# Kernel optimization log

Hardware: AMD Instinct MI355X
Metric: run time of the kernel (lower is better)

## Reference

```python
import jax, jax.numpy as jnp
import numpy as np

K = 3   # kernel_size
D = 1   # dilation
G = 8   # groups
BN_EPS = 1e-5


def setup_inputs() -> dict:
    key = jax.random.key(0)
    ks = jax.random.split(key, 8)
    N, C, H, W = 8, 64, 256, 256
    k2 = K * K
    x = jax.random.normal(ks[0], (N, C, H, W), jnp.float32)
    conv_w = jax.random.normal(ks[1], (G * k2, C), jnp.float32) * (2.0 / C) ** 0.5
    bn_gamma = jnp.ones((G * k2,), jnp.float32)
    bn_beta = jnp.zeros((G * k2,), jnp.float32)
    bn_mean = jax.random.normal(ks[2], (G * k2,), jnp.float32) * 0.01
    bn_var = jax.random.uniform(ks[3], (G * k2,), jnp.float32, 0.5, 1.5)
    lamb_l = jax.random.normal(ks[4], (C,), jnp.float32) * 0.1
    lamb_h = jax.random.normal(ks[5], (C,), jnp.float32) * 0.1
    inside_all = jax.random.normal(ks[6], (C, 1, 1), jnp.float32) * 0.1
    return {"x": x, "conv_w": conv_w, "bn_gamma": bn_gamma, "bn_beta": bn_beta,
            "bn_mean": bn_mean, "bn_var": bn_var, "lamb_l": lamb_l,
            "lamb_h": lamb_h, "inside_all": inside_all}


def reference(x, conv_w, bn_gamma, bn_beta, bn_mean, bn_var, lamb_l, lamb_h, inside_all):
    N, C, H, W = x.shape
    k2 = K * K
    # ap: adaptive avg pool to (1,1) -> (N, C)
    pooled = x.mean(axis=(2, 3))
    # 1x1 conv on a 1x1 map == matmul; then eval-mode BatchNorm
    lf = pooled @ conv_w.T                                   # (N, G*k2)
    lf = (lf - bn_mean) * (bn_gamma / jnp.sqrt(bn_var + BN_EPS)) + bn_beta
    lf = jnp.tanh(lf).reshape(N, G, 1, k2, 1)                # (N, G, 1, k2, 1)
    # im2col/unfold with reflection padding; ordering matches torch (C, kh, kw)
    p = D * (K - 1) // 2
    xp = jnp.pad(x, ((0, 0), (0, 0), (p, p), (p, p)), mode="reflect")
    patches = jnp.stack(
        [xp[:, :, i * D:i * D + H, j * D:j * D + W] for i in range(K) for j in range(K)],
        axis=2,
    )                                                        # (N, C, k2, H, W)
    xu = patches.reshape(N, G, C // G, k2, H * W)
    low_part = jnp.sum(xu * lf, axis=3).reshape(N, C, H, W)  # per-pixel dynamic filter
    # DSA: gap pools to (1,1)
    gap = x.mean(axis=(2, 3), keepdims=True)                 # (N, C, 1, 1)
    out_low = (low_part * (inside_all + 1.0) - inside_all * gap) * lamb_l[None, :, None, None]
    out_high = x * (lamb_h[None, :, None, None] + 1.0)
    return out_low + out_high
```

## Files before the change

kernel.cpp:

```cpp
#include <hip/hip_runtime.h>
#include <math.h>

#define NN 8
#define CC 64
#define HH 256
#define WW 256
#define GG 8
#define K2 9
#define OC 72
#define BN_EPS 1e-5f

typedef float f4 __attribute__((ext_vector_type(4)));

__global__ __launch_bounds__(1024) void pool_kernel(const float* __restrict__ x,
                                                    float* __restrict__ pooled) {
    int nc = blockIdx.x;
    const f4* p4 = (const f4*)(x + (size_t)nc * (HH * WW));
    float s = 0.f;
#pragma unroll 4
    for (int i = threadIdx.x; i < (HH * WW) / 4; i += 1024) {
        f4 v = p4[i];
        s += (v.x + v.y) + (v.z + v.w);
    }
    for (int off = 32; off > 0; off >>= 1) s += __shfl_down(s, off, 64);
    __shared__ float smem[16];
    int lane = threadIdx.x & 63, wid = threadIdx.x >> 6;
    if (lane == 0) smem[wid] = s;
    __syncthreads();
    if (threadIdx.x < 16) {
        float t = smem[threadIdx.x];
        for (int off = 8; off > 0; off >>= 1) t += __shfl_down(t, off, 64);
        if (threadIdx.x == 0) pooled[nc] = t * (1.0f / (HH * WW));
    }
}

__global__ __launch_bounds__(256) void lf_kernel(const float* __restrict__ pooled,
                                                 const float* __restrict__ conv_w,
                                                 const float* __restrict__ gamma,
                                                 const float* __restrict__ beta,
                                                 const float* __restrict__ mean,
                                                 const float* __restrict__ var,
                                                 float* __restrict__ lf) {
    int j = blockIdx.x * blockDim.x + threadIdx.x;
    if (j >= NN * OC) return;
    int n = j / OC, oc = j % OC;
    const float* pw = conv_w + oc * CC;
    const float* pp = pooled + n * CC;
    float acc = 0.f;
#pragma unroll 8
    for (int c = 0; c < CC; ++c) acc += pp[c] * pw[c];
    float inv = gamma[oc] / sqrtf(var[oc] + BN_EPS);
    lf[j] = tanhf((acc - mean[oc]) * inv + beta[oc]);
}

__global__ __launch_bounds__(256) void main_kernel(const float* __restrict__ x,
                                                   const float* __restrict__ lf,
                                                   const float* __restrict__ pooled,
                                                   const float* __restrict__ lamb_l,
                                                   const float* __restrict__ lamb_h,
                                                   const float* __restrict__ ia,
                                                   float* __restrict__ out) {
    const int bid  = (int)(blockIdx.x & 7) * ((NN * CC * (HH / 32)) >> 3)
                   + (int)(blockIdx.x >> 3);
    const int wid  = threadIdx.x >> 6;
    const int lane = threadIdx.x & 63;
    const int nc   = bid >> 3;
    const int r0   = ((bid & 7) << 5) + (wid << 3);
    const int c    = nc & (CC - 1);
    const int n    = nc >> 6;
    const int g    = c >> 3;

    const float* lw = lf + (n * OC + g * K2);
    const float w00 = lw[0], w01 = lw[1], w02 = lw[2];
    const float w10 = lw[3], w11 = lw[4], w12 = lw[5];
    const float w20 = lw[6], w21 = lw[7], w22 = lw[8];
    const float ll    = lamb_l[c];
    const float lh1   = lamb_h[c] + 1.0f;
    const float iav   = ia[c];
    const float scale = iav + 1.0f;
    const float bias  = -iav * pooled[nc];

    const float* base = x + (size_t)nc * (HH * WW);

    f4    v[10];
    float L[10], R[10];
#pragma unroll
    for (int i = 0; i < 10; ++i) {
        int r = r0 - 1 + i;
        r = (r < 0) ? 1 : ((r > HH - 1) ? HH - 2 : r);
        v[i] = ((const f4*)(base + (size_t)r * WW))[lane];
    }
#pragma unroll
    for (int i = 0; i < 10; ++i) {
        L[i] = __shfl_up(v[i].w, 1, 64);   if (lane == 0)  L[i] = v[i].y;
        R[i] = __shfl_down(v[i].x, 1, 64); if (lane == 63) R[i] = v[i].z;
    }

    float* outbase = out + (size_t)nc * (HH * WW);
#pragma unroll
    for (int j = 0; j < 8; ++j) {
        const float t[6] = {L[j],   v[j].x,   v[j].y,   v[j].z,   v[j].w,   R[j]};
        const float m[6] = {L[j+1], v[j+1].x, v[j+1].y, v[j+1].z, v[j+1].w, R[j+1]};
        const float b[6] = {L[j+2], v[j+2].x, v[j+2].y, v[j+2].z, v[j+2].w, R[j+2]};
        f4 o;
#pragma unroll
        for (int k = 0; k < 4; ++k) {
            float acc = w00 * t[k] + w01 * t[k + 1] + w02 * t[k + 2]
                      + w10 * m[k] + w11 * m[k + 1] + w12 * m[k + 2]
                      + w20 * b[k] + w21 * b[k + 1] + w22 * b[k + 2];
            o[k] = ll * (scale * acc + bias) + lh1 * m[k + 1];
        }
        __builtin_nontemporal_store(o, ((f4*)(outbase + (size_t)(r0 + j) * WW)) + lane);
    }
}

extern "C" void kernel_launch(void* const* d_in, const int* in_sizes, int n_in,
                              void* d_out, int out_size, void* d_ws, size_t ws_size,
                              hipStream_t stream) {
    const float* x      = (const float*)d_in[0];
    const float* conv_w = (const float*)d_in[1];
    const float* gamma  = (const float*)d_in[2];
    const float* beta   = (const float*)d_in[3];
    const float* mean   = (const float*)d_in[4];
    const float* var    = (const float*)d_in[5];
    const float* lamb_l = (const float*)d_in[6];
    const float* lamb_h = (const float*)d_in[7];
    const float* ia     = (const float*)d_in[8];
    float* out = (float*)d_out;

    float* pooled = (float*)d_ws;
    float* lf     = pooled + NN * CC;

    pool_kernel<<<NN * CC, 1024, 0, stream>>>(x, pooled);
    lf_kernel<<<(NN * OC + 255) / 256, 256, 0, stream>>>(pooled, conv_w, gamma, beta,
                                                         mean, var, lf);
    main_kernel<<<NN * CC * (HH / 32), 256, 0, stream>>>(x, lf, pooled, lamb_l, lamb_h,
                                                         ia, out);
}
```

Measured before the change: 264.7 us.

## Fuse pool, filter generation and dynamic conv into one kernel with grid barrier

```diff
diff --git a/kernel.cpp b/kernel.cpp
--- a/kernel.cpp
+++ b/kernel.cpp
@@ -5,112 +5,130 @@
 #define CC 64
 #define HH 256
 #define WW 256
-#define GG 8
 #define K2 9
 #define OC 72
 #define BN_EPS 1e-5f
+#define NBLK (NN * CC * 2)
 
 typedef float f4 __attribute__((ext_vector_type(4)));
 
-__global__ __launch_bounds__(1024) void pool_kernel(const float* __restrict__ x,
-                                                    float* __restrict__ pooled) {
-    int nc = blockIdx.x;
-    const f4* p4 = (const f4*)(x + (size_t)nc * (HH * WW));
-    float s = 0.f;
-#pragma unroll 4
-    for (int i = threadIdx.x; i < (HH * WW) / 4; i += 1024) {
-        f4 v = p4[i];
-        s += (v.x + v.y) + (v.z + v.w);
-    }
-    for (int off = 32; off > 0; off >>= 1) s += __shfl_down(s, off, 64);
-    __shared__ float smem[16];
-    int lane = threadIdx.x & 63, wid = threadIdx.x >> 6;
-    if (lane == 0) smem[wid] = s;
-    __syncthreads();
-    if (threadIdx.x < 16) {
-        float t = smem[threadIdx.x];
-        for (int off = 8; off > 0; off >>= 1) t += __shfl_down(t, off, 64);
-        if (threadIdx.x == 0) pooled[nc] = t * (1.0f / (HH * WW));
-    }
-}
-
-__global__ __launch_bounds__(256) void lf_kernel(const float* __restrict__ pooled,
-                                                 const float* __restrict__ conv_w,
-                                                 const float* __restrict__ gamma,
-                                                 const float* __restrict__ beta,
-                                                 const float* __restrict__ mean,
-                                                 const float* __restrict__ var,
-                                                 float* __restrict__ lf) {
-    int j = blockIdx.x * blockDim.x + threadIdx.x;
-    if (j >= NN * OC) return;
-    int n = j / OC, oc = j % OC;
-    const float* pw = conv_w + oc * CC;
-    const float* pp = pooled + n * CC;
-    float acc = 0.f;
-#pragma unroll 8
-    for (int c = 0; c < CC; ++c) acc += pp[c] * pw[c];
-    float inv = gamma[oc] / sqrtf(var[oc] + BN_EPS);
-    lf[j] = tanhf((acc - mean[oc]) * inv + beta[oc]);
-}
-
-__global__ __launch_bounds__(256) void main_kernel(const float* __restrict__ x,
-                                                   const float* __restrict__ lf,
-                                                   const float* __restrict__ pooled,
-                                                   const float* __restrict__ lamb_l,
-                                                   const float* __restrict__ lamb_h,
-                                                   const float* __restrict__ ia,
-                                                   float* __restrict__ out) {
-    const int bid  = (int)(blockIdx.x & 7) * ((NN * CC * (HH / 32)) >> 3)
-                   + (int)(blockIdx.x >> 3);
+__global__ __launch_bounds__(256, 4) void fused_kernel(
+    const float* __restrict__ x,
+    const float* __restrict__ conv_w,
+    const float* __restrict__ gamma,
+    const float* __restrict__ beta,
+    const float* __restrict__ mean,
+    const float* __restrict__ var,
+    const float* __restrict__ lamb_l,
+    const float* __restrict__ lamb_h,
+    const float* __restrict__ ia,
+    float* __restrict__ out,
+    float* __restrict__ ws,
+    unsigned* __restrict__ sync)
+{
+    const int b    = blockIdx.x;
+    const int nc   = b >> 1;
+    const int half = b & 1;
+    const int lane = threadIdx.x & 63;
     const int wid  = threadIdx.x >> 6;
-    const int lane = threadIdx.x & 63;
-    const int nc   = bid >> 3;
-    const int r0   = ((bid & 7) << 5) + (wid << 3);
     const int c    = nc & (CC - 1);
     const int n    = nc >> 6;
     const int g    = c >> 3;
 
-    const float* lw = lf + (n * OC + g * K2);
-    const float w00 = lw[0], w01 = lw[1], w02 = lw[2];
-    const float w10 = lw[3], w11 = lw[4], w12 = lw[5];
-    const float w20 = lw[6], w21 = lw[7], w22 = lw[8];
+    const float* base  = x + (size_t)nc * (HH * WW);
+    const f4*    hbase = (const f4*)(base + half * (HH / 2) * WW);
+
+    float s = 0.f;
+#pragma unroll 8
+    for (int i = threadIdx.x; i < (HH / 2) * WW / 4; i += 256) {
+        f4 v = hbase[i];
+        s += (v.x + v.y) + (v.z + v.w);
+    }
+    for (int off = 32; off > 0; off >>= 1) s += __shfl_down(s, off, 64);
+    __shared__ float red[4];
+    if (lane == 0) red[wid] = s;
+    __syncthreads();
+    if (threadIdx.x == 0) {
+        float t = (red[0] + red[1]) + (red[2] + red[3]);
+        __hip_atomic_store(&ws[b], t, __ATOMIC_RELEASE, __HIP_MEMORY_SCOPE_AGENT);
+    }
+    __syncthreads();
+
+    if (threadIdx.x == 0) {
+        unsigned prev = __hip_atomic_fetch_add(&sync[0], 1u, __ATOMIC_ACQ_REL,
+                                               __HIP_MEMORY_SCOPE_AGENT);
+        if (prev == NBLK - 1)
+            __hip_atomic_store(&sync[1], 1u, __ATOMIC_RELEASE,
+                               __HIP_MEMORY_SCOPE_AGENT);
+        while (__hip_atomic_load(&sync[1], __ATOMIC_ACQUIRE,
+                                 __HIP_MEMORY_SCOPE_AGENT) == 0u) {
+            __builtin_amdgcn_s_sleep(8);
+        }
+    }
+    __syncthreads();
+
+    __shared__ float pl[CC];
+    __shared__ float lfs[K2];
+    if (threadIdx.x < CC) {
+        float a0 = __hip_atomic_load(&ws[2 * (n * CC + threadIdx.x)],
+                                     __ATOMIC_ACQUIRE, __HIP_MEMORY_SCOPE_AGENT);
+        float a1 = __hip_atomic_load(&ws[2 * (n * CC + threadIdx.x) + 1],
+                                     __ATOMIC_ACQUIRE, __HIP_MEMORY_SCOPE_AGENT);
+        pl[threadIdx.x] = (a0 + a1) * (1.0f / (HH * WW));
+    }
+    __syncthreads();
+    if (threadIdx.x < K2) {
+        int oc = g * K2 + threadIdx.x;
+        const float* pw = conv_w + oc * CC;
+        float acc = 0.f;
+#pragma unroll
+        for (int cc2 = 0; cc2 < CC; ++cc2) acc += pl[cc2] * pw[cc2];
+        float inv = gamma[oc] / sqrtf(var[oc] + BN_EPS);
+        lfs[threadIdx.x] = tanhf((acc - mean[oc]) * inv + beta[oc]);
+    }
+    __syncthreads();
+
+    const float w00 = lfs[0], w01 = lfs[1], w02 = lfs[2];
+    const float w10 = lfs[3], w11 = lfs[4], w12 = lfs[5];
+    const float w20 = lfs[6], w21 = lfs[7], w22 = lfs[8];
     const float ll    = lamb_l[c];
     const float lh1   = lamb_h[c] + 1.0f;
     const float iav   = ia[c];
     const float scale = iav + 1.0f;
-    const float bias  = -iav * pooled[nc];
-
-    const float* base = x + (size_t)nc * (HH * WW);
-
-    f4    v[10];
-    float L[10], R[10];
-#pragma unroll
-    for (int i = 0; i < 10; ++i) {
-        int r = r0 - 1 + i;
-        r = (r < 0) ? 1 : ((r > HH - 1) ? HH - 2 : r);
-        v[i] = ((const f4*)(base + (size_t)r * WW))[lane];
-    }
-#pragma unroll
-    for (int i = 0; i < 10; ++i) {
-        L[i] = __shfl_up(v[i].w, 1, 64);   if (lane == 0)  L[i] = v[i].y;
-        R[i] = __shfl_down(v[i].x, 1, 64); if (lane == 63) R[i] = v[i].z;
-    }
+    const float bias  = -iav * pl[c];
 
     float* outbase = out + (size_t)nc * (HH * WW);
+
+    for (int chunk = 0; chunk < 4; ++chunk) {
+        const int r0 = half * (HH / 2) + chunk * 32 + wid * 8;
+        f4    v[10];
+        float L[10], R[10];
 #pragma unroll
-    for (int j = 0; j < 8; ++j) {
-        const float t[6] = {L[j],   v[j].x,   v[j].y,   v[j].z,   v[j].w,   R[j]};
-        const float m[6] = {L[j+1], v[j+1].x, v[j+1].y, v[j+1].z, v[j+1].w, R[j+1]};
-        const float b[6] = {L[j+2], v[j+2].x, v[j+2].y, v[j+2].z, v[j+2].w, R[j+2]};
-        f4 o;
+        for (int i = 0; i < 10; ++i) {
+            int r = r0 - 1 + i;
+            r = (r < 0) ? 1 : ((r > HH - 1) ? HH - 2 : r);
+            v[i] = ((const f4*)(base + (size_t)r * WW))[lane];
+        }
 #pragma unroll
-        for (int k = 0; k < 4; ++k) {
-            float acc = w00 * t[k] + w01 * t[k + 1] + w02 * t[k + 2]
-                      + w10 * m[k] + w11 * m[k + 1] + w12 * m[k + 2]
-                      + w20 * b[k] + w21 * b[k + 1] + w22 * b[k + 2];
-            o[k] = ll * (scale * acc + bias) + lh1 * m[k + 1];
+        for (int i = 0; i < 10; ++i) {
+            L[i] = __shfl_up(v[i].w, 1, 64);   if (lane == 0)  L[i] = v[i].y;
+            R[i] = __shfl_down(v[i].x, 1, 64); if (lane == 63) R[i] = v[i].z;
         }
-        __builtin_nontemporal_store(o, ((f4*)(outbase + (size_t)(r0 + j) * WW)) + lane);
+#pragma unroll
+        for (int j = 0; j < 8; ++j) {
+            const float t[6]  = {L[j],   v[j].x,   v[j].y,   v[j].z,   v[j].w,   R[j]};
+            const float m[6]  = {L[j+1], v[j+1].x, v[j+1].y, v[j+1].z, v[j+1].w, R[j+1]};
+            const float bb[6] = {L[j+2], v[j+2].x, v[j+2].y, v[j+2].z, v[j+2].w, R[j+2]};
+            f4 o;
+#pragma unroll
+            for (int k = 0; k < 4; ++k) {
+                float acc = w00 * t[k]  + w01 * t[k + 1]  + w02 * t[k + 2]
+                          + w10 * m[k]  + w11 * m[k + 1]  + w12 * m[k + 2]
+                          + w20 * bb[k] + w21 * bb[k + 1] + w22 * bb[k + 2];
+                o[k] = ll * (scale * acc + bias) + lh1 * m[k + 1];
+            }
+            __builtin_nontemporal_store(o, ((f4*)(outbase + (size_t)(r0 + j) * WW)) + lane);
+        }
     }
 }
 
@@ -127,13 +145,10 @@
     const float* lamb_h = (const float*)d_in[7];
     const float* ia     = (const float*)d_in[8];
     float* out = (float*)d_out;
+    float* ws  = (float*)d_ws;
+    unsigned* sync = (unsigned*)(ws + NBLK);
 
-    float* pooled = (float*)d_ws;
-    float* lf     = pooled + NN * CC;
-
-    pool_kernel<<<NN * CC, 1024, 0, stream>>>(x, pooled);
-    lf_kernel<<<(NN * OC + 255) / 256, 256, 0, stream>>>(pooled, conv_w, gamma, beta,
-                                                         mean, var, lf);
-    main_kernel<<<NN * CC * (HH / 32), 256, 0, stream>>>(x, lf, pooled, lamb_l, lamb_h,
-                                                         ia, out);
+    hipMemsetAsync(sync, 0, 2 * sizeof(unsigned), stream);
+    fused_kernel<<<NBLK, 256, 0, stream>>>(x, conv_w, gamma, beta, mean, var,
+                                           lamb_l, lamb_h, ia, out, ws, sync);
 }
```

Measured after the change: 444.9 us. 68.1% more time.
